# Optimization experiments

Measured on AMD Instinct MI355X. Metric: run time of the kernel, lower is better.

Reference implementation:

```python
import jax, jax.numpy as jnp
import numpy as np

NUM_HEADS = 12


def get_rel_pos(q_size, k_size, rel_pos):
    # rel_pos: (2*max(q,k)-1, C). Here q_size==k_size so no interpolation needed.
    q_coords = jnp.arange(q_size)[:, None] * max(k_size / q_size, 1.0)
    k_coords = jnp.arange(k_size)[None, :] * max(q_size / k_size, 1.0)
    rel = (q_coords - k_coords) + (k_size - 1) * max(q_size / k_size, 1.0)
    return rel_pos[rel.astype(jnp.int32)]  # (q_size, k_size, C)


def add_decomposed_rel_pos(attn, q, rel_pos_h, rel_pos_w, q_size, k_size):
    q_h, q_w = q_size
    k_h, k_w = k_size
    Rh = get_rel_pos(q_h, k_h, rel_pos_h)  # (q_h,k_h,C)
    Rw = get_rel_pos(q_w, k_w, rel_pos_w)  # (q_w,k_w,C)
    B, _, C = q.shape  # B = num_heads * batch
    r_q = q.reshape(B, q_h, q_w, C)
    rel_h = jnp.einsum('bhwc,hkc->bhwk', r_q, Rh)  # (B,q_h,q_w,k_h)
    rel_w = jnp.einsum('bhwc,wkc->bhwk', r_q, Rw)  # (B,q_h,q_w,k_w)
    attn = attn.reshape(B, q_h, q_w, k_h, k_w)
    attn = attn + rel_h[:, :, :, :, None] + rel_w[:, :, :, None, :]
    return attn.reshape(B, q_h * q_w, k_h * k_w)


def setup_inputs() -> dict:
    key = jax.random.key(0)
    ks = jax.random.split(key, 7)
    B, H, W, dim = 128, 14, 14, 768
    head_dim = dim // NUM_HEADS
    return {
        'x': jax.random.normal(ks[0], (B, H, W, dim), dtype=jnp.float32),
        'qkv_w': jax.random.normal(ks[1], (dim, 3 * dim), dtype=jnp.float32) * 0.02,
        'qkv_b': jax.random.normal(ks[2], (3 * dim,), dtype=jnp.float32) * 0.02,
        'proj_w': jax.random.normal(ks[3], (dim, dim), dtype=jnp.float32) * 0.02,
        'proj_b': jax.random.normal(ks[4], (dim,), dtype=jnp.float32) * 0.02,
        'rel_pos_h': jax.random.normal(ks[5], (2 * H - 1, head_dim), dtype=jnp.float32) * 0.02,
        'rel_pos_w': jax.random.normal(ks[6], (2 * W - 1, head_dim), dtype=jnp.float32) * 0.02,
    }


def reference(x, qkv_w, qkv_b, proj_w, proj_b, rel_pos_h, rel_pos_w):
    B, H, W, dim = x.shape
    nh = NUM_HEADS
    hd = dim // nh
    scale = hd ** -0.5
    L = H * W
    # qkv projection: (B,H,W,3*dim) -> (3, nh*B, L, hd)
    qkv = x.reshape(B, L, dim) @ qkv_w + qkv_b
    qkv = qkv.reshape(B, L, 3, nh, hd)
    qkv = jnp.transpose(qkv, (2, 3, 0, 1, 4)).reshape(3, nh * B, L, hd)
    q, k, v = qkv[0], qkv[1], qkv[2]
    attn = jnp.einsum('bqc,bkc->bqk', q * scale, k)  # (nh*B, L, L)
    attn = add_decomposed_rel_pos(attn, q, rel_pos_h, rel_pos_w, (H, W), (H, W))
    attn = jax.nn.softmax(attn, axis=-1)
    out = jnp.einsum('bqk,bkc->bqc', attn, v)  # (nh*B, L, hd)
    out = out.reshape(nh, B, H, W, hd)
    out = jnp.transpose(out, (1, 2, 3, 0, 4)).reshape(B, H, W, dim)
    return out @ proj_w + proj_b
```

## Files before the change

### kernel.cpp

```cpp
#include <hip/hip_runtime.h>
#include <stdint.h>

typedef unsigned short u16;
typedef __bf16 bf16x8 __attribute__((ext_vector_type(8)));
typedef u16 u16x8 __attribute__((ext_vector_type(8)));
typedef float f32x4 __attribute__((ext_vector_type(4)));

#define MFMA16(a,b,c) __builtin_amdgcn_mfma_f32_16x16x32_bf16((a),(b),(c),0,0,0)
#define GLOAD16(gp, lp) __builtin_amdgcn_global_load_lds( \
    (const __attribute__((address_space(1))) void*)(gp), \
    (__attribute__((address_space(3))) void*)(lp), 16, 0, 0)

__device__ __forceinline__ u16 f2bf(float f) {
  union { float f; uint32_t u; } v; v.f = f;
  return (u16)((v.u + 0x7FFFu + ((v.u >> 16) & 1u)) >> 16);
}
__device__ __forceinline__ float bits2f(uint32_t u) {
  union { uint32_t u; float f; } v; v.u = u; return v.f;
}
__device__ __forceinline__ uint32_t cvtpk(float lo, float hi) {
  uint32_t r;
  asm("v_cvt_pk_bf16_f32 %0, %1, %2" : "=v"(r) : "v"(lo), "v"(hi));
  return r;
}
__device__ __forceinline__ int4 pack8(const u16* v) {
  int4 r;
  r.x = (int)((uint32_t)v[0] | ((uint32_t)v[1] << 16));
  r.y = (int)((uint32_t)v[2] | ((uint32_t)v[3] << 16));
  r.z = (int)((uint32_t)v[4] | ((uint32_t)v[5] << 16));
  r.w = (int)((uint32_t)v[6] | ((uint32_t)v[7] << 16));
  return r;
}

__global__ void k_cvt(const float* __restrict__ in, u16* __restrict__ out, int n4) {
  int i = blockIdx.x * 256 + threadIdx.x;
  int stride = gridDim.x * 256;
  for (; i < n4; i += stride) {
    float4 v = reinterpret_cast<const float4*>(in)[i];
    ushort4 o;
    o.x = f2bf(v.x); o.y = f2bf(v.y); o.z = f2bf(v.z); o.w = f2bf(v.w);
    reinterpret_cast<ushort4*>(out)[i] = o;
  }
}

__global__ void k_transpose(const float* __restrict__ in, u16* __restrict__ out, int R, int C) {
  __shared__ float t[32][33];
  int tx = threadIdx.x & 31, ty = threadIdx.x >> 5;
  int c0 = blockIdx.x * 32, r0 = blockIdx.y * 32;
  #pragma unroll
  for (int i = 0; i < 4; i++)
    t[ty + i*8][tx] = in[(size_t)(r0 + ty + i*8) * C + (c0 + tx)];
  __syncthreads();
  #pragma unroll
  for (int i = 0; i < 4; i++)
    out[(size_t)(c0 + ty + i*8) * R + (r0 + tx)] = f2bf(t[tx][ty + i*8]);
}

__global__ __launch_bounds__(512, 2) void k_qkv256(
    const u16* __restrict__ A, const u16* __restrict__ BT, const float* __restrict__ bias,
    u16* __restrict__ qo, u16* __restrict__ ko, u16* __restrict__ vo)
{
  __shared__ u16 SMEM[65536];

  int bid0 = blockIdx.x;
  int xcd = bid0 & 7, idx = bid0 >> 3;
  int base = (xcd < 2) ? xcd * 111 : 2 * 111 + (xcd - 2) * 110;
  int wgid = base + idx;
  int mt = wgid / 9, nt = wgid - (wgid / 9) * 9;

  int tid = threadIdx.x, lane = tid & 63, w = tid >> 6;
  int g = lane >> 4, c4 = lane & 15;
  int wr = w >> 2, wc = w & 3;

  int srow = lane >> 2;
  int pslot = (lane & 3) ^ ((lane >> 3) & 3);
  int cidA = w * 2;

  const u16* pA1 = A + (size_t)(mt * 256 + cidA * 16 + srow) * 768 + pslot * 8;
  const u16* pA2 = pA1 + 16 * 768;
  const u16* pB1 = BT + (size_t)(nt * 256 + cidA * 16 + srow) * 768 + pslot * 8;
  const u16* pB2 = pB1 + 16 * 768;

  int rsel = g ^ ((c4 >> 1) & 3);
  int aoff = wr * 4096 + c4 * 32 + rsel * 8;
  int boff = wc * 2048 + c4 * 32 + rsel * 8;

  f32x4 acc[8][4];
  f32x4 z4 = {0.f, 0.f, 0.f, 0.f};
  #pragma unroll
  for (int f = 0; f < 8; f++)
    #pragma unroll
    for (int fc = 0; fc < 4; fc++) acc[f][fc] = z4;

  #pragma unroll
  for (int kk = 0; kk < 3; kk++) {
    u16* dA = SMEM + kk * 8192;
    GLOAD16(pA1 + kk * 32, dA + cidA * 512);
    GLOAD16(pA2 + kk * 32, dA + (cidA + 1) * 512);
    u16* dB = SMEM + 32768 + kk * 8192;
    GLOAD16(pB1 + kk * 32, dB + cidA * 512);
    GLOAD16(pB2 + kk * 32, dB + (cidA + 1) * 512);
  }
  asm volatile("s_waitcnt vmcnt(8)" ::: "memory");
  __builtin_amdgcn_s_barrier();

  for (int k = 0; k < 24; ++k) {
    const u16* As = SMEM + (k & 3) * 8192;
    const u16* Bs = SMEM + 32768 + (k & 3) * 8192;
    bf16x8 bfr[4], afr[4];
    #pragma unroll
    for (int fc = 0; fc < 4; fc++) bfr[fc] = *(const bf16x8*)(Bs + boff + fc * 512);
    #pragma unroll
    for (int f = 0; f < 4; f++) afr[f] = *(const bf16x8*)(As + aoff + f * 512);
    if (k < 21) {
      u16* d = SMEM + ((k + 3) & 3) * 8192;
      GLOAD16(pA1 + (k + 3) * 32, d + cidA * 512);
      GLOAD16(pA2 + (k + 3) * 32, d + (cidA + 1) * 512);
      asm volatile("s_waitcnt vmcnt(6)" ::: "memory");
    } else if (k == 21) {
      asm volatile("s_waitcnt vmcnt(0)" ::: "memory");
    }
    __builtin_amdgcn_s_barrier();
    __builtin_amdgcn_s_setprio(1);
    #pragma unroll
    for (int f = 0; f < 4; f++)
      #pragma unroll
      for (int fc = 0; fc < 4; fc++)
        acc[f][fc] = MFMA16(afr[f], bfr[fc], acc[f][fc]);
    __builtin_amdgcn_s_setprio(0);

    #pragma unroll
    for (int f = 0; f < 4; f++) afr[f] = *(const bf16x8*)(As + aoff + (4 + f) * 512);
    if (k < 21) {
      u16* d = SMEM + 32768 + ((k + 3) & 3) * 8192;
      GLOAD16(pB1 + (k + 3) * 32, d + cidA * 512);
      GLOAD16(pB2 + (k + 3) * 32, d + (cidA + 1) * 512);
      asm volatile("s_waitcnt vmcnt(6)" ::: "memory");
    }
    __builtin_amdgcn_s_barrier();
    __builtin_amdgcn_s_setprio(1);
    #pragma unroll
    for (int f = 0; f < 4; f++)
      #pragma unroll
      for (int fc = 0; fc < 4; fc++)
        acc[4 + f][fc] = MFMA16(afr[f], bfr[fc], acc[4 + f][fc]);
    __builtin_amdgcn_s_setprio(0);
  }

  int i3 = nt / 3;
  u16* dst = (i3 == 0) ? qo : (i3 == 1) ? ko : vo;
  int head = (nt - i3 * 3) * 4 + wc;
  float bsv[4];
  #pragma unroll
  for (int fc = 0; fc < 4; fc++) bsv[fc] = bias[nt * 256 + wc * 64 + fc * 16 + c4];

  int mbase = mt * 256 + wr * 128 + g * 4;
  #pragma unroll
  for (int f = 0; f < 8; f++) {
    #pragma unroll
    for (int j = 0; j < 4; j++) {
      int mm = mbase + f * 16 + j;
      int bb2 = mm / 196, ll = mm - bb2 * 196;
      size_t ro = (size_t)((head * 128 + bb2) * 196 + ll) * 64;
      #pragma unroll
      for (int fc = 0; fc < 4; fc++)
        dst[ro + fc * 16 + c4] = f2bf(acc[f][fc][j] + bsv[fc]);
    }
  }
}

__global__ __launch_bounds__(256, 2) void k_proj256(
    const u16* __restrict__ A, const u16* __restrict__ BT, const float* __restrict__ bias,
    float* __restrict__ out)
{
  __shared__ u16 SMEM[32768];

  int bid0 = blockIdx.x;
  int bid = (bid0 & 7) * 147 + (bid0 >> 3);
  int nt = bid % 6, mt = bid / 6;

  int tid = threadIdx.x, lane = tid & 63, w = tid >> 6;
  int g = lane >> 4, c4 = lane & 15;
  int wr = w >> 1, wc = w & 1;

  int srow = lane >> 2;
  int pslot = (lane & 3) ^ ((lane >> 3) & 3);
  int cidA = w * 2;

  const u16* pA1 = A + (size_t)(mt * 128 + cidA * 16 + srow) * 768 + pslot * 8;
  const u16* pA2 = pA1 + 16 * 768;
  const u16* pB1 = BT + (size_t)(nt * 128 + cidA * 16 + srow) * 768 + pslot * 8;
  const u16* pB2 = pB1 + 16 * 768;

  int rsel = g ^ ((c4 >> 1) & 3);
  int aoff = wr * 2048 + c4 * 32 + rsel * 8;
  int boff = wc * 2048 + c4 * 32 + rsel * 8;

  f32x4 acc[4][4];
  f32x4 z4 = {0.f, 0.f, 0.f, 0.f};
  #pragma unroll
  for (int f = 0; f < 4; f++)
    #pragma unroll
    for (int fc = 0; fc < 4; fc++) acc[f][fc] = z4;

  #pragma unroll
  for (int kk = 0; kk < 3; kk++) {
    u16* dA = SMEM + kk * 4096;
    GLOAD16(pA1 + kk * 32, dA + cidA * 512);
    GLOAD16(pA2 + kk * 32, dA + (cidA + 1) * 512);
    u16* dB = SMEM + 16384 + kk * 4096;
    GLOAD16(pB1 + kk * 32, dB + cidA * 512);
    GLOAD16(pB2 + kk * 32, dB + (cidA + 1) * 512);
  }
  asm volatile("s_waitcnt vmcnt(8)" ::: "memory");
  __builtin_amdgcn_s_barrier();

  for (int k = 0; k < 24; ++k) {
    const u16* As = SMEM + (k & 3) * 4096;
    const u16* Bs = SMEM + 16384 + (k & 3) * 4096;
    bf16x8 bfr[4], afr[4];
    #pragma unroll
    for (int fc = 0; fc < 4; fc++) bfr[fc] = *(const bf16x8*)(Bs + boff + fc * 512);
    #pragma unroll
    for (int f = 0; f < 4; f++) afr[f] = *(const bf16x8*)(As + aoff + f * 512);
    if (k < 21) {
      u16* dA = SMEM + ((k + 3) & 3) * 4096;
      GLOAD16(pA1 + (k + 3) * 32, dA + cidA * 512);
      GLOAD16(pA2 + (k + 3) * 32, dA + (cidA + 1) * 512);
      u16* dB = SMEM + 16384 + ((k + 3) & 3) * 4096;
      GLOAD16(pB1 + (k + 3) * 32, dB + cidA * 512);
      GLOAD16(pB2 + (k + 3) * 32, dB + (cidA + 1) * 512);
      asm volatile("s_waitcnt vmcnt(8)" ::: "memory");
    } else if (k == 21) {
      asm volatile("s_waitcnt vmcnt(4)" ::: "memory");
    } else if (k == 22) {
      asm volatile("s_waitcnt vmcnt(0)" ::: "memory");
    }
    __builtin_amdgcn_s_barrier();
    __builtin_amdgcn_s_setprio(1);
    #pragma unroll
    for (int f = 0; f < 4; f++)
      #pragma unroll
      for (int fc = 0; fc < 4; fc++)
        acc[f][fc] = MFMA16(afr[f], bfr[fc], acc[f][fc]);
    __builtin_amdgcn_s_setprio(0);
    __builtin_amdgcn_s_barrier();
  }

  #pragma unroll
  for (int fc = 0; fc < 4; fc++) {
    int n0 = nt * 128 + wc * 64 + fc * 16 + c4;
    float bs = bias[n0];
    #pragma unroll
    for (int fr = 0; fr < 4; fr++)
      #pragma unroll
      for (int j = 0; j < 4; j++) {
        int m = mt * 128 + wr * 64 + fr * 16 + g * 4 + j;
        out[(size_t)m * 768 + n0] = acc[fr][fc][j] + bs;
      }
  }
}

#define VP 232
__global__ __launch_bounds__(256, 2) void k_attn(
    const u16* __restrict__ Q, const u16* __restrict__ Kg, const u16* __restrict__ Vg,
    const u16* __restrict__ RPH, const u16* __restrict__ RPW, u16* __restrict__ Ows)
{
  __shared__ u16 K64[208 * 64];
  __shared__ u16 Krel[208 * 40];
  __shared__ u16 VT[64 * VP];
  __shared__ u16 Qrel[4][16 * 40];

  int bh = blockIdx.x;
  int hh = bh >> 7, bb = bh & 127;
  int tid = threadIdx.x, lane = tid & 63, w = tid >> 6;
  int g = lane >> 4, c4 = lane & 15;

  const u16* kbase = Kg + (size_t)bh * 12544;
  const u16* vbase = Vg + (size_t)bh * 12544;
  const u16* qbase = Q + (size_t)bh * 12544;

  for (int ch = tid; ch < 1664; ch += 256) {
    int row = ch >> 3, s = ch & 7;
    u16 outv[8];
    if (row < 196) {
      u16x8 v = *(const u16x8*)(kbase + row * 64 + s * 8);
      #pragma unroll
      for (int e = 0; e < 8; e++)
        outv[e] = f2bf(bits2f((uint32_t)v[e] << 16) * 0.125f);
    } else {
      #pragma unroll
      for (int e = 0; e < 8; e++) outv[e] = 0;
    }
    *(int4*)(K64 + row * 64 + ((s ^ (row & 7)) * 8)) = pack8(outv);
  }
  if (tid < 208) {
    int k = tid;
    int kh = k / 14, kw2 = k - kh * 14;
    #pragma unroll
    for (int s = 0; s < 5; s++) {
      u16 vals[8];
      #pragma unroll
      for (int e = 0; e < 8; e++) {
        int c = s * 8 + e;
        u16 x = 0;
        if (k < 196) {
          if (c == kh) x = 0x3F80;
          else if (c == 14 + kw2) x = 0x3F80;
        } else {
          if (c == 28) x = 0x3F80;
        }
        vals[e] = x;
      }
      *(int4*)(Krel + k * 40 + s * 8) = pack8(vals);
    }
  }
  for (int i = tid; i < 2048; i += 256) {
    int chn = i >> 5, c = 192 + (i & 31);
    if (c >= 196 && c < VP) VT[chn * VP + c] = 0;
  }
  for (int ch2 = tid; ch2 < 784; ch2 += 256) {
    int kp = ch2 >> 3, cb = ch2 & 7;
    int key = kp * 2, cz = cb * 8;
    u16x8 a = *(const u16x8*)(vbase + key * 64 + cz);
    u16x8 b2 = *(const u16x8*)(vbase + (key + 1) * 64 + cz);
    int kk = key & 31;
    int colp = (key >> 5) * 32 + ((kk & 15) >> 2) * 8 + (kk & 3) + ((kk >> 4) << 2);
    #pragma unroll
    for (int j = 0; j < 8; j++) {
      uint32_t pk = (uint32_t)a[j] | ((uint32_t)b2[j] << 16);
      *(uint32_t*)(VT + (cz + j) * VP + colp) = pk;
    }
  }
  __syncthreads();

  int t1 = 16 + c4; if (t1 > 26) t1 = 26;
  bf16x8 rh00 = *(const bf16x8*)(RPH + c4 * 64 + g * 8);
  bf16x8 rh01 = *(const bf16x8*)(RPH + c4 * 64 + 32 + g * 8);
  bf16x8 rh10 = *(const bf16x8*)(RPH + t1 * 64 + g * 8);
  bf16x8 rh11 = *(const bf16x8*)(RPH + t1 * 64 + 32 + g * 8);
  bf16x8 rw00 = *(const bf16x8*)(RPW + c4 * 64 + g * 8);
  bf16x8 rw01 = *(const bf16x8*)(RPW + c4 * 64 + 32 + g * 8);
  bf16x8 rw10 = *(const bf16x8*)(RPW + t1 * 64 + g * 8);
  bf16x8 rw11 = *(const bf16x8*)(RPW + t1 * 64 + 32 + g * 8);

  f32x4 z4 = {0.f, 0.f, 0.f, 0.f};

  for (int qt = w; qt < 13; qt += 4) {
    int qi = qt * 16 + c4;
    int qrow = qi > 195 ? 195 : qi;
    bf16x8 qa0 = *(const bf16x8*)(qbase + qrow * 64 + g * 8);
    bf16x8 qa1 = *(const bf16x8*)(qbase + qrow * 64 + 32 + g * 8);

    u16* Qr = (u16*)Qrel[w];
    {
      int4 zz = {0, 0, 0, 0};
      *(int4*)(Qr + lane * 8) = zz;
      if (lane < 16) *(int4*)(Qr + 512 + lane * 8) = zz;
      if (g == 0) Qr[c4 * 40 + 28] = f2bf(-30000.f);
    }

    int qh = qi / 14;
    int qwv = qi - qh * 14;

    f32x4 e0 = MFMA16(rh00, qa0, z4); e0 = MFMA16(rh01, qa1, e0);
    f32x4 e1 = MFMA16(rh10, qa0, z4); e1 = MFMA16(rh11, qa1, e1);
    #pragma unroll
    for (int tt = 0; tt < 2; tt++) {
      f32x4 e = tt ? e1 : e0;
      #pragma unroll
      for (int j = 0; j < 4; j++) {
        int t = tt * 16 + 4 * g + j;
        int kh = qh + 13 - t;
        if ((unsigned)kh <= 13u) Qr[c4 * 40 + kh] = f2bf(e[j]);
      }
    }
    f32x4 f0 = MFMA16(rw00, qa0, z4); f0 = MFMA16(rw01, qa1, f0);
    f32x4 f1 = MFMA16(rw10, qa0, z4); f1 = MFMA16(rw11, qa1, f1);
    #pragma unroll
    for (int tt = 0; tt < 2; tt++) {
      f32x4 e = tt ? f1 : f0;
      #pragma unroll
      for (int j = 0; j < 4; j++) {
        int t = tt * 16 + 4 * g + j;
        int kw3 = qwv + 13 - t;
        if ((unsigned)kw3 <= 13u) Qr[c4 * 40 + 14 + kw3] = f2bf(e[j]);
      }
    }

    bf16x8 qrelB = *(const bf16x8*)(Qr + c4 * 40 + g * 8);

    f32x4 St[13];
    #pragma unroll
    for (int i = 0; i < 13; i++) {
      int key = i * 16 + c4;
      const u16* kr = K64 + key * 64;
      int sw = key & 7;
      bf16x8 kb0 = *(const bf16x8*)(kr + ((g ^ sw) * 8));
      bf16x8 kb1 = *(const bf16x8*)(kr + (((4 + g) ^ sw) * 8));
      f32x4 acc = MFMA16(kb0, qa0, z4);
      acc = MFMA16(kb1, qa1, acc);
      bf16x8 krl = *(const bf16x8*)(Krel + key * 40 + g * 8);
      St[i] = MFMA16(krl, qrelB, acc);
    }

    float mx = -3.0e38f;
    #pragma unroll
    for (int i = 0; i < 13; i++)
      #pragma unroll
      for (int j = 0; j < 4; j++) mx = fmaxf(mx, St[i][j]);
    mx = fmaxf(mx, __shfl_xor(mx, 16));
    mx = fmaxf(mx, __shfl_xor(mx, 32));

    float ls = 0.f;
    f32x4 O[4] = {z4, z4, z4, z4};
    #pragma unroll
    for (int p = 0; p < 7; p++) {
      float pe[8];
      #pragma unroll
      for (int j2 = 0; j2 < 4; j2++) { pe[j2] = __expf(St[2 * p][j2] - mx); ls += pe[j2]; }
      if (p < 6) {
        #pragma unroll
        for (int j2 = 0; j2 < 4; j2++) { pe[4 + j2] = __expf(St[2 * p + 1][j2] - mx); ls += pe[4 + j2]; }
      } else {
        #pragma unroll
        for (int j2 = 0; j2 < 4; j2++) pe[4 + j2] = 0.f;
      }
      union { uint32_t u[4]; bf16x8 v; } pb;
      pb.u[0] = cvtpk(pe[0], pe[1]);
      pb.u[1] = cvtpk(pe[2], pe[3]);
      pb.u[2] = cvtpk(pe[4], pe[5]);
      pb.u[3] = cvtpk(pe[6], pe[7]);
      #pragma unroll
      for (int ct = 0; ct < 4; ct++) {
        bf16x8 va = *(const bf16x8*)(VT + (ct * 16 + c4) * VP + p * 32 + g * 8);
        O[ct] = MFMA16(va, pb.v, O[ct]);
      }
    }
    ls += __shfl_xor(ls, 16);
    ls += __shfl_xor(ls, 32);

    if (qi < 196) {
      float inv = 1.f / ls;
      size_t obase = (size_t)(bb * 196 + qi) * 768 + hh * 64;
      #pragma unroll
      for (int ct = 0; ct < 4; ct++) {
        uint32_t o0 = cvtpk(O[ct][0] * inv, O[ct][1] * inv);
        uint32_t o1 = cvtpk(O[ct][2] * inv, O[ct][3] * inv);
        uint2 ov = {o0, o1};
        *(uint2*)(Ows + obase + ct * 16 + g * 4) = ov;
      }
    }
  }
}

extern "C" void kernel_launch(void* const* d_in, const int* in_sizes, int n_in,
                              void* d_out, int out_size, void* d_ws, size_t ws_size,
                              hipStream_t stream) {
  (void)in_sizes; (void)n_in; (void)out_size; (void)ws_size;
  const float* x      = (const float*)d_in[0];
  const float* qkv_w  = (const float*)d_in[1];
  const float* qkv_b  = (const float*)d_in[2];
  const float* proj_w = (const float*)d_in[3];
  const float* proj_b = (const float*)d_in[4];
  const float* rph    = (const float*)d_in[5];
  const float* rpw    = (const float*)d_in[6];
  float* out = (float*)d_out;
  char* ws = (char*)d_ws;

  u16* xb   = (u16*)(ws);
  u16* wT   = (u16*)(ws + 38535168);
  u16* pT   = (u16*)(ws + 42074112);
  u16* rphb = (u16*)(ws + 43253760);
  u16* rpwb = (u16*)(ws + 43257856);
  u16* qws  = (u16*)(ws + 43261952);
  u16* kws  = (u16*)(ws + 81797120);
  u16* vws  = (u16*)(ws + 120332288);
  u16* Ows  = xb;

  k_cvt<<<2048, 256, 0, stream>>>(x, xb, 4816896);
  k_cvt<<<2, 256, 0, stream>>>(rph, rphb, 432);
  k_cvt<<<2, 256, 0, stream>>>(rpw, rpwb, 432);
  k_transpose<<<dim3(72, 24), 256, 0, stream>>>(qkv_w, wT, 768, 2304);
  k_transpose<<<dim3(24, 24), 256, 0, stream>>>(proj_w, pT, 768, 768);
  k_qkv256<<<882, 512, 0, stream>>>(xb, wT, qkv_b, qws, kws, vws);
  k_attn<<<1536, 256, 0, stream>>>(qws, kws, vws, rphb, rpwb, Ows);
  k_proj256<<<1176, 256, 0, stream>>>(Ows, pT, proj_b, out);
}
```

Measured before the change: 263.8 us.

## Software-pipeline GEMM fragment loads, use exp2 softmax, prefetch Q tiles

The QKV and projection GEMM main loops are restructured so the LDS fragments for step k+1 are read while the MFMAs of step k run, with register double buffering, one barrier per step and a deeper prefetch distance. The attention kernel folds log2(e) into the K scale and the relative-position tables so softmax can call exp2f instead of __expf. It also prefetches the next Q tile's fragments into registers and changes the V transpose loop's index mapping. These aim to hide LDS latency, cut per-step barriers and trim exponent cost, in exchange for higher register pressure.

After: 270.2 us. +2.4%, slower.

```diff
diff --git a/kernel.cpp b/kernel.cpp
--- a/kernel.cpp
+++ b/kernel.cpp
@@ -1,5 +1,6 @@
 #include <hip/hip_runtime.h>
 #include <stdint.h>
+#include <math.h>
 
 typedef unsigned short u16;
 typedef __bf16 bf16x8 __attribute__((ext_vector_type(8)));
@@ -32,13 +33,14 @@
   return r;
 }
 
-__global__ void k_cvt(const float* __restrict__ in, u16* __restrict__ out, int n4) {
+__global__ void k_cvt(const float* __restrict__ in, u16* __restrict__ out, int n4, float scale) {
   int i = blockIdx.x * 256 + threadIdx.x;
   int stride = gridDim.x * 256;
   for (; i < n4; i += stride) {
     float4 v = reinterpret_cast<const float4*>(in)[i];
     ushort4 o;
-    o.x = f2bf(v.x); o.y = f2bf(v.y); o.z = f2bf(v.z); o.w = f2bf(v.w);
+    o.x = f2bf(v.x * scale); o.y = f2bf(v.y * scale);
+    o.z = f2bf(v.z * scale); o.w = f2bf(v.w * scale);
     reinterpret_cast<ushort4*>(out)[i] = o;
   }
 }
@@ -54,6 +56,24 @@
   #pragma unroll
   for (int i = 0; i < 4; i++)
     out[(size_t)(c0 + ty + i*8) * R + (r0 + tx)] = f2bf(t[tx][ty + i*8]);
+}
+
+__device__ __forceinline__ void rd_frags12(const u16* As_, const u16* Bs_, int aoff, int boff,
+                                           bf16x8 (&b)[4], bf16x8 (&aA)[4], bf16x8 (&aB)[4]) {
+  #pragma unroll
+  for (int fc = 0; fc < 4; fc++) b[fc] = *(const bf16x8*)(Bs_ + boff + fc * 512);
+  #pragma unroll
+  for (int f = 0; f < 4; f++) {
+    aA[f] = *(const bf16x8*)(As_ + aoff + f * 512);
+    aB[f] = *(const bf16x8*)(As_ + aoff + (4 + f) * 512);
+  }
+}
+__device__ __forceinline__ void rd_frags8(const u16* As_, const u16* Bs_, int aoff, int boff,
+                                          bf16x8 (&b)[4], bf16x8 (&a)[4]) {
+  #pragma unroll
+  for (int fc = 0; fc < 4; fc++) b[fc] = *(const bf16x8*)(Bs_ + boff + fc * 512);
+  #pragma unroll
+  for (int f = 0; f < 4; f++) a[f] = *(const bf16x8*)(As_ + aoff + f * 512);
 }
 
 __global__ __launch_bounds__(512, 2) void k_qkv256(
@@ -104,48 +124,49 @@
   asm volatile("s_waitcnt vmcnt(8)" ::: "memory");
   __builtin_amdgcn_s_barrier();
 
-  for (int k = 0; k < 24; ++k) {
-    const u16* As = SMEM + (k & 3) * 8192;
-    const u16* Bs = SMEM + 32768 + (k & 3) * 8192;
-    bf16x8 bfr[4], afr[4];
-    #pragma unroll
-    for (int fc = 0; fc < 4; fc++) bfr[fc] = *(const bf16x8*)(Bs + boff + fc * 512);
-    #pragma unroll
-    for (int f = 0; f < 4; f++) afr[f] = *(const bf16x8*)(As + aoff + f * 512);
-    if (k < 21) {
-      u16* d = SMEM + ((k + 3) & 3) * 8192;
-      GLOAD16(pA1 + (k + 3) * 32, d + cidA * 512);
-      GLOAD16(pA2 + (k + 3) * 32, d + (cidA + 1) * 512);
-      asm volatile("s_waitcnt vmcnt(6)" ::: "memory");
-    } else if (k == 21) {
-      asm volatile("s_waitcnt vmcnt(0)" ::: "memory");
-    }
-    __builtin_amdgcn_s_barrier();
-    __builtin_amdgcn_s_setprio(1);
-    #pragma unroll
-    for (int f = 0; f < 4; f++)
-      #pragma unroll
-      for (int fc = 0; fc < 4; fc++)
-        acc[f][fc] = MFMA16(afr[f], bfr[fc], acc[f][fc]);
-    __builtin_amdgcn_s_setprio(0);
-
-    #pragma unroll
-    for (int f = 0; f < 4; f++) afr[f] = *(const bf16x8*)(As + aoff + (4 + f) * 512);
-    if (k < 21) {
-      u16* d = SMEM + 32768 + ((k + 3) & 3) * 8192;
-      GLOAD16(pB1 + (k + 3) * 32, d + cidA * 512);
-      GLOAD16(pB2 + (k + 3) * 32, d + (cidA + 1) * 512);
-      asm volatile("s_waitcnt vmcnt(6)" ::: "memory");
-    }
-    __builtin_amdgcn_s_barrier();
-    __builtin_amdgcn_s_setprio(1);
-    #pragma unroll
-    for (int f = 0; f < 4; f++)
-      #pragma unroll
-      for (int fc = 0; fc < 4; fc++)
-        acc[4 + f][fc] = MFMA16(afr[f], bfr[fc], acc[4 + f][fc]);
-    __builtin_amdgcn_s_setprio(0);
-  }
+  bf16x8 cb0[4], ca0[4], cd0[4], cb1[4], ca1[4], cd1[4];
+  rd_frags12(SMEM, SMEM + 32768, aoff, boff, cb0, ca0, cd0);
+  {
+    u16* dA = SMEM + 3 * 8192;
+    GLOAD16(pA1 + 3 * 32, dA + cidA * 512);
+    GLOAD16(pA2 + 3 * 32, dA + (cidA + 1) * 512);
+    u16* dB = SMEM + 32768 + 3 * 8192;
+    GLOAD16(pB1 + 3 * 32, dB + cidA * 512);
+    GLOAD16(pB2 + 3 * 32, dB + (cidA + 1) * 512);
+  }
+  asm volatile("s_waitcnt vmcnt(6)" ::: "memory");
+
+#define QKV_REGION(K, CB, CAA, CAB, NB, NAA, NAB)                           \
+  __builtin_amdgcn_s_barrier();                                             \
+  if ((K) < 20) {                                                           \
+    u16* dA_ = SMEM + (((K) + 4) & 3) * 8192;                               \
+    GLOAD16(pA1 + ((K) + 4) * 32, dA_ + cidA * 512);                        \
+    GLOAD16(pA2 + ((K) + 4) * 32, dA_ + (cidA + 1) * 512);                  \
+    u16* dB_ = SMEM + 32768 + (((K) + 4) & 3) * 8192;                       \
+    GLOAD16(pB1 + ((K) + 4) * 32, dB_ + cidA * 512);                        \
+    GLOAD16(pB2 + ((K) + 4) * 32, dB_ + (cidA + 1) * 512);                  \
+  }                                                                         \
+  __builtin_amdgcn_s_setprio(1);                                            \
+  _Pragma("unroll") for (int f_ = 0; f_ < 4; f_++)                          \
+    _Pragma("unroll") for (int fc_ = 0; fc_ < 4; fc_++)                     \
+      acc[f_][fc_] = MFMA16(CAA[f_], CB[fc_], acc[f_][fc_]);                \
+  if ((K) < 23)                                                             \
+    rd_frags12(SMEM + (((K) + 1) & 3) * 8192,                               \
+               SMEM + 32768 + (((K) + 1) & 3) * 8192, aoff, boff,           \
+               NB, NAA, NAB);                                               \
+  _Pragma("unroll") for (int f_ = 0; f_ < 4; f_++)                          \
+    _Pragma("unroll") for (int fc_ = 0; fc_ < 4; fc_++)                     \
+      acc[4 + f_][fc_] = MFMA16(CAB[f_], CB[fc_], acc[4 + f_][fc_]);        \
+  __builtin_amdgcn_s_setprio(0);                                            \
+  if ((K) < 20)       { asm volatile("s_waitcnt vmcnt(6)" ::: "memory"); }  \
+  else if ((K) == 20) { asm volatile("s_waitcnt vmcnt(2)" ::: "memory"); }  \
+  else if ((K) == 21) { asm volatile("s_waitcnt vmcnt(0)" ::: "memory"); }
+
+  for (int kk = 0; kk < 24; kk += 2) {
+    QKV_REGION(kk,     cb0, ca0, cd0, cb1, ca1, cd1)
+    QKV_REGION(kk + 1, cb1, ca1, cd1, cb0, ca0, cd0)
+  }
+#undef QKV_REGION
 
   int i3 = nt / 3;
   u16* dst = (i3 == 0) ? qo : (i3 == 1) ? ko : vo;
@@ -215,37 +236,45 @@
   asm volatile("s_waitcnt vmcnt(8)" ::: "memory");
   __builtin_amdgcn_s_barrier();
 
-  for (int k = 0; k < 24; ++k) {
-    const u16* As = SMEM + (k & 3) * 4096;
-    const u16* Bs = SMEM + 16384 + (k & 3) * 4096;
-    bf16x8 bfr[4], afr[4];
-    #pragma unroll
-    for (int fc = 0; fc < 4; fc++) bfr[fc] = *(const bf16x8*)(Bs + boff + fc * 512);
-    #pragma unroll
-    for (int f = 0; f < 4; f++) afr[f] = *(const bf16x8*)(As + aoff + f * 512);
-    if (k < 21) {
-      u16* dA = SMEM + ((k + 3) & 3) * 4096;
-      GLOAD16(pA1 + (k + 3) * 32, dA + cidA * 512);
-      GLOAD16(pA2 + (k + 3) * 32, dA + (cidA + 1) * 512);
-      u16* dB = SMEM + 16384 + ((k + 3) & 3) * 4096;
-      GLOAD16(pB1 + (k + 3) * 32, dB + cidA * 512);
-      GLOAD16(pB2 + (k + 3) * 32, dB + (cidA + 1) * 512);
-      asm volatile("s_waitcnt vmcnt(8)" ::: "memory");
-    } else if (k == 21) {
-      asm volatile("s_waitcnt vmcnt(4)" ::: "memory");
-    } else if (k == 22) {
-      asm volatile("s_waitcnt vmcnt(0)" ::: "memory");
-    }
-    __builtin_amdgcn_s_barrier();
-    __builtin_amdgcn_s_setprio(1);
-    #pragma unroll
-    for (int f = 0; f < 4; f++)
-      #pragma unroll
-      for (int fc = 0; fc < 4; fc++)
-        acc[f][fc] = MFMA16(afr[f], bfr[fc], acc[f][fc]);
-    __builtin_amdgcn_s_setprio(0);
-    __builtin_amdgcn_s_barrier();
-  }
+  bf16x8 cbE[4], caE[4], cbO[4], caO[4];
+  rd_frags8(SMEM, SMEM + 16384, aoff, boff, cbE, caE);
+  {
+    u16* dA = SMEM + 3 * 4096;
+    GLOAD16(pA1 + 3 * 32, dA + cidA * 512);
+    GLOAD16(pA2 + 3 * 32, dA + (cidA + 1) * 512);
+    u16* dB = SMEM + 16384 + 3 * 4096;
+    GLOAD16(pB1 + 3 * 32, dB + cidA * 512);
+    GLOAD16(pB2 + 3 * 32, dB + (cidA + 1) * 512);
+  }
+  asm volatile("s_waitcnt vmcnt(6)" ::: "memory");
+
+#define PROJ_REGION(K, CB, CA, NB, NA)                                      \
+  __builtin_amdgcn_s_barrier();                                             \
+  if ((K) < 20) {                                                           \
+    u16* dA_ = SMEM + (((K) + 4) & 3) * 4096;                               \
+    GLOAD16(pA1 + ((K) + 4) * 32, dA_ + cidA * 512);                        \
+    GLOAD16(pA2 + ((K) + 4) * 32, dA_ + (cidA + 1) * 512);                  \
+    u16* dB_ = SMEM + 16384 + (((K) + 4) & 3) * 4096;                       \
+    GLOAD16(pB1 + ((K) + 4) * 32, dB_ + cidA * 512);                        \
+    GLOAD16(pB2 + ((K) + 4) * 32, dB_ + (cidA + 1) * 512);                  \
+  }                                                                         \
+  __builtin_amdgcn_s_setprio(1);                                            \
+  _Pragma("unroll") for (int f_ = 0; f_ < 4; f_++)                          \
+    _Pragma("unroll") for (int fc_ = 0; fc_ < 4; fc_++)                     \
+      acc[f_][fc_] = MFMA16(CA[f_], CB[fc_], acc[f_][fc_]);                 \
+  if ((K) < 23)                                                             \
+    rd_frags8(SMEM + (((K) + 1) & 3) * 4096,                                \
+              SMEM + 16384 + (((K) + 1) & 3) * 4096, aoff, boff, NB, NA);   \
+  __builtin_amdgcn_s_setprio(0);                                            \
+  if ((K) < 20)       { asm volatile("s_waitcnt vmcnt(6)" ::: "memory"); }  \
+  else if ((K) == 20) { asm volatile("s_waitcnt vmcnt(2)" ::: "memory"); }  \
+  else if ((K) == 21) { asm volatile("s_waitcnt vmcnt(0)" ::: "memory"); }
+
+  for (int kk = 0; kk < 24; kk += 2) {
+    PROJ_REGION(kk,     cbE, caE, cbO, caO)
+    PROJ_REGION(kk + 1, cbO, caO, cbE, caE)
+  }
+#undef PROJ_REGION
 
   #pragma unroll
   for (int fc = 0; fc < 4; fc++) {
@@ -280,6 +309,7 @@
   const u16* vbase = Vg + (size_t)bh * 12544;
   const u16* qbase = Q + (size_t)bh * 12544;
 
+  const float KSC = 0.18033688011f;
   for (int ch = tid; ch < 1664; ch += 256) {
     int row = ch >> 3, s = ch & 7;
     u16 outv[8];
@@ -287,7 +317,7 @@
       u16x8 v = *(const u16x8*)(kbase + row * 64 + s * 8);
       #pragma unroll
       for (int e = 0; e < 8; e++)
-        outv[e] = f2bf(bits2f((uint32_t)v[e] << 16) * 0.125f);
+        outv[e] = f2bf(bits2f((uint32_t)v[e] << 16) * KSC);
     } else {
       #pragma unroll
       for (int e = 0; e < 8; e++) outv[e] = 0;
@@ -320,7 +350,7 @@
     if (c >= 196 && c < VP) VT[chn * VP + c] = 0;
   }
   for (int ch2 = tid; ch2 < 784; ch2 += 256) {
-    int kp = ch2 >> 3, cb = ch2 & 7;
+    int kp = ch2 % 98, cb = ch2 / 98;
     int key = kp * 2, cz = cb * 8;
     u16x8 a = *(const u16x8*)(vbase + key * 64 + cz);
     u16x8 b2 = *(const u16x8*)(vbase + (key + 1) * 64 + cz);
@@ -346,11 +376,20 @@
 
   f32x4 z4 = {0.f, 0.f, 0.f, 0.f};
 
+  int qi0 = w * 16 + c4;
+  int qr0 = qi0 > 195 ? 195 : qi0;
+  bf16x8 qa0 = *(const bf16x8*)(qbase + qr0 * 64 + g * 8);
+  bf16x8 qa1 = *(const bf16x8*)(qbase + qr0 * 64 + 32 + g * 8);
+
   for (int qt = w; qt < 13; qt += 4) {
     int qi = qt * 16 + c4;
-    int qrow = qi > 195 ? 195 : qi;
-    bf16x8 qa0 = *(const bf16x8*)(qbase + qrow * 64 + g * 8);
-    bf16x8 qa1 = *(const bf16x8*)(qbase + qrow * 64 + 32 + g * 8);
+    bf16x8 nq0, nq1;
+    int qn = qt + 4;
+    if (qn < 13) {
+      int qrn = qn * 16 + c4; if (qrn > 195) qrn = 195;
+      nq0 = *(const bf16x8*)(qbase + qrn * 64 + g * 8);
+      nq1 = *(const bf16x8*)(qbase + qrn * 64 + 32 + g * 8);
+    }
 
     u16* Qr = (u16*)Qrel[w];
     {
@@ -418,10 +457,10 @@
     for (int p = 0; p < 7; p++) {
       float pe[8];
       #pragma unroll
-      for (int j2 = 0; j2 < 4; j2++) { pe[j2] = __expf(St[2 * p][j2] - mx); ls += pe[j2]; }
+      for (int j2 = 0; j2 < 4; j2++) { pe[j2] = exp2f(St[2 * p][j2] - mx); ls += pe[j2]; }
       if (p < 6) {
         #pragma unroll
-        for (int j2 = 0; j2 < 4; j2++) { pe[4 + j2] = __expf(St[2 * p + 1][j2] - mx); ls += pe[4 + j2]; }
+        for (int j2 = 0; j2 < 4; j2++) { pe[4 + j2] = exp2f(St[2 * p + 1][j2] - mx); ls += pe[4 + j2]; }
       } else {
         #pragma unroll
         for (int j2 = 0; j2 < 4; j2++) pe[4 + j2] = 0.f;
@@ -451,6 +490,7 @@
         *(uint2*)(Ows + obase + ct * 16 + g * 4) = ov;
       }
     }
+    qa0 = nq0; qa1 = nq1;
   }
 }
 
@@ -478,9 +518,10 @@
   u16* vws  = (u16*)(ws + 120332288);
   u16* Ows  = xb;
 
-  k_cvt<<<2048, 256, 0, stream>>>(x, xb, 4816896);
-  k_cvt<<<2, 256, 0, stream>>>(rph, rphb, 432);
-  k_cvt<<<2, 256, 0, stream>>>(rpw, rpwb, 432);
+  const float LOG2E = 1.44269504f;
+  k_cvt<<<2048, 256, 0, stream>>>(x, xb, 4816896, 1.0f);
+  k_cvt<<<2, 256, 0, stream>>>(rph, rphb, 432, LOG2E);
+  k_cvt<<<2, 256, 0, stream>>>(rpw, rpwb, 432, LOG2E);
   k_transpose<<<dim3(72, 24), 256, 0, stream>>>(qkv_w, wT, 768, 2304);
   k_transpose<<<dim3(24, 24), 256, 0, stream>>>(proj_w, pT, 768, 768);
   k_qkv256<<<882, 512, 0, stream>>>(xb, wT, qkv_b, qws, kws, vws);
```
